# Kernel tuning notes

Measured on AMD Instinct MI355X. Metric: run time of the kernel, lower is better.

## Reference

```python
import jax, jax.numpy as jnp
import numpy as np

KNN, D, CONV_NUM, LEVELS, POOL_RATIO = 4, 64, 6, 3, 8
QN, RFN, NS, H, W = 4, 32, 4, 64, 64
CN = LEVELS * CONV_NUM  # 18 = 3 embed levels x 6 correlation variants


def instance_norm(x, eps=1e-5):
    # InstanceNorm2d(affine=False): normalize each (sample, channel) over H,W (biased var)
    m = x.mean(axis=(-2, -1), keepdims=True)
    v = x.var(axis=(-2, -1), keepdims=True)
    return (x - m) * jax.lax.rsqrt(v + eps)


def conv2d(x, w, b):
    y = jax.lax.conv_general_dilated(x, w, (1, 1), 'SAME', dimension_numbers=('NCHW', 'OIHW', 'NCHW'))
    return y + b[None, :, None, None]


def conv1x1x1(x, w, b):
    # Conv3d kernel 1x1x1 == pure channel mixing; x: (qn,C,ns,h,w), w: (Cout,Cin)
    return jnp.einsum('qcshw,oc->qoshw', x, w) + b[None, :, None, None, None]


def head(x, w1, b1, w2, b2, w3, b3):
    x = jax.nn.relu(conv2d(x, w1, b1))
    x = jax.nn.relu(conv2d(x, w2, b2))
    return conv2d(x, w3, b3)


def setup_inputs():
    key = jax.random.key(0)
    ks = iter(jax.random.split(key, 64))
    def rn(shape, scale=0.05):
        return jax.random.normal(next(ks), shape, jnp.float32) * scale
    inp = {'corr': jax.random.normal(next(ks), (QN, RFN, NS, CN, H, W), jnp.float32)}
    inp['scale_conv_w1'] = rn((D, CN * KNN)); inp['scale_conv_b1'] = rn((D,))
    inp['scale_conv_w2'] = rn((D, D)); inp['scale_conv_b2'] = rn((D,))
    inp['score_conv_w1'] = rn((D, LEVELS * KNN)); inp['score_conv_b1'] = rn((D,))
    inp['score_conv_w2'] = rn((D, D)); inp['score_conv_b2'] = rn((D,))
    for name, cout in (('scale_pred', 1), ('offset_pred', 2), ('score_pred', 1)):
        inp[name + '_w1'] = rn((D, D, 3, 3)); inp[name + '_b1'] = rn((D,))
        inp[name + '_w2'] = rn((D, D, 3, 3)); inp[name + '_b2'] = rn((D,))
        inp[name + '_w3'] = rn((cout, D, 3, 3)); inp[name + '_b3'] = rn((cout,))
    return inp


def _maps(corr, scale_conv_w1, scale_conv_b1, scale_conv_w2, scale_conv_b2,
          score_conv_w1, score_conv_b1, score_conv_w2, score_conv_b2,
          scale_pred_w1, scale_pred_b1, scale_pred_w2, scale_pred_b2, scale_pred_w3, scale_pred_b3,
          offset_pred_w1, offset_pred_b1, offset_pred_w2, offset_pred_b2, offset_pred_w3, offset_pred_b3,
          score_pred_w1, score_pred_b1, score_pred_w2, score_pred_b2, score_pred_w3, score_pred_b3):
    qn, rfn, ns, cn, h, w = corr.shape
    corr_n = instance_norm(corr)                         # score_norm
    # per-(scale,position) matching score per reference -> knn refs
    ref_score = corr_n.mean(axis=3)                      # qn,rfn,ns,h,w
    rs = jnp.moveaxis(ref_score, 1, -1)                  # qn,ns,h,w,rfn
    _, top_idx = jax.lax.top_k(rs, KNN)                  # qn,ns,h,w,knn
    feat = jnp.transpose(corr_n, (0, 2, 4, 5, 1, 3))     # qn,ns,h,w,rfn,cn
    knn_feat = jnp.take_along_axis(feat, top_idx[..., None], axis=4)  # qn,ns,h,w,knn,cn
    x_scale = jnp.transpose(knn_feat.reshape(qn, ns, h, w, KNN * cn), (0, 4, 1, 2, 3))  # qn,72,ns,h,w
    lvl = corr_n.reshape(qn, rfn, ns, LEVELS, CONV_NUM, h, w).mean(axis=4)  # per-level score
    lvl = jnp.transpose(lvl, (0, 2, 4, 5, 1, 3))         # qn,ns,h,w,rfn,3
    knn_lvl = jnp.take_along_axis(lvl, top_idx[..., None], axis=4)
    x_score = jnp.transpose(knn_lvl.reshape(qn, ns, h, w, KNN * LEVELS), (0, 4, 1, 2, 3))  # qn,12,ns,h,w
    xs = conv1x1x1(jax.nn.relu(conv1x1x1(x_scale, scale_conv_w1, scale_conv_b1)), scale_conv_w2, scale_conv_b2).max(axis=2)
    xc = conv1x1x1(jax.nn.relu(conv1x1x1(x_score, score_conv_w1, score_conv_b1)), score_conv_w2, score_conv_b2).max(axis=2)
    scales = head(xs, scale_pred_w1, scale_pred_b1, scale_pred_w2, scale_pred_b2, scale_pred_w3, scale_pred_b3)
    offsets = head(xc, offset_pred_w1, offset_pred_b1, offset_pred_w2, offset_pred_b2, offset_pred_w3, offset_pred_b3)
    scores = head(xc, score_pred_w1, score_pred_b1, score_pred_w2, score_pred_b2, score_pred_w3, score_pred_b3)
    return scores, scales, offsets


def reference(corr, scale_conv_w1, scale_conv_b1, scale_conv_w2, scale_conv_b2,
              score_conv_w1, score_conv_b1, score_conv_w2, score_conv_b2,
              scale_pred_w1, scale_pred_b1, scale_pred_w2, scale_pred_b2, scale_pred_w3, scale_pred_b3,
              offset_pred_w1, offset_pred_b1, offset_pred_w2, offset_pred_b2, offset_pred_w3, offset_pred_b3,
              score_pred_w1, score_pred_b1, score_pred_w2, score_pred_b2, score_pred_w3, score_pred_b3):
    scores, scales, offsets = _maps(corr, scale_conv_w1, scale_conv_b1, scale_conv_w2, scale_conv_b2,
                                    score_conv_w1, score_conv_b1, score_conv_w2, score_conv_b2,
                                    scale_pred_w1, scale_pred_b1, scale_pred_w2, scale_pred_b2, scale_pred_w3, scale_pred_b3,
                                    offset_pred_w1, offset_pred_b1, offset_pred_w2, offset_pred_b2, offset_pred_w3, offset_pred_b3,
                                    score_pred_w1, score_pred_b1, score_pred_w2, score_pred_b2, score_pred_w3, score_pred_b3)
    # parse_detection: argmax + advanced-index gathers
    qn = scores.shape[0]; h, w = scores.shape[-2:]
    sid = jnp.argmax(scores.reshape(qn, -1), axis=1)
    sy, sx = sid // w, sid % w
    q = jnp.arange(qn)
    off = offsets[q, :, sy, sx]                          # qn,2
    pos = (jnp.stack([sx, sy], -1).astype(scores.dtype) + off + 0.5) * POOL_RATIO - 0.5
    scl = 2.0 ** scales[q, 0, sy, sx]
    return pos, scl, scores, scales, offsets
```

## Files before the change

kernel.cpp:

```cpp
#include <hip/hip_runtime.h>

#define HW 4096

__global__ __launch_bounds__(256) void k_statsrs(
    const float* __restrict__ corr, float* __restrict__ scl,
    float* __restrict__ shf, float* __restrict__ rs,
    const float* __restrict__ p0, const float* __restrict__ p1,
    const float* __restrict__ p2, const float* __restrict__ p3,
    const float* __restrict__ p4, const float* __restrict__ p5,
    float* __restrict__ wT, const float* __restrict__ w1s,
    const float* __restrict__ w2s, const float* __restrict__ w1c,
    const float* __restrict__ w2c, float* __restrict__ wm) {
  int t = threadIdx.x;
  if (blockIdx.x >= 512) {
    int b = blockIdx.x - 512;
    if (b < 96) {
      int arr = b >> 4;
      int chunk = b & 15;
      const float* src = (arr == 0) ? p0
                         : (arr == 1) ? p1
                         : (arr == 2) ? p2
                         : (arr == 3) ? p3
                         : (arr == 4) ? p4 : p5;
      float* dst = wT + arr * 36864;
#pragma unroll
      for (int i = 0; i < 9; i++) {
        int e = chunk * 2304 + i * 256 + t;
        int oc = e / 576;
        int rem = e - oc * 576;
        dst[rem * 64 + oc] = src[e];
      }
    } else {
      int i = (b - 96) * 256 + t;
      if (i < 4608) {
        int c = i >> 6, o = i & 63;
        wm[i] = w1s[o * 72 + c];
      } else if (i < 8704) {
        int j = i - 4608;
        int c = j >> 6, o = j & 63;
        wm[i] = w2s[o * 64 + c];
      } else if (i < 9472) {
        int j = i - 8704;
        int c = j >> 6, o = j & 63;
        wm[i] = w1c[o * 12 + c];
      } else if (i < 13568) {
        int j = i - 9472;
        int c = j >> 6, o = j & 63;
        wm[i] = w2c[o * 64 + c];
      }
    }
    return;
  }
  int g = blockIdx.x;
  const float4* p = (const float4*)(corr + (size_t)g * 18 * HW);

  float s[18], s2[18];
#pragma unroll
  for (int c = 0; c < 18; c++) { s[c] = 0.f; s2[c] = 0.f; }
#pragma unroll
  for (int c = 0; c < 18; c++) {
#pragma unroll
    for (int i = 0; i < 4; i++) {
      float4 v = p[(c << 10) + (i << 8) + t];
      s[c] += v.x + v.y + v.z + v.w;
      s2[c] += v.x * v.x + v.y * v.y + v.z * v.z + v.w * v.w;
    }
  }
#pragma unroll
  for (int c = 0; c < 18; c++) {
#pragma unroll
    for (int o = 1; o < 64; o <<= 1) {
      s[c] += __shfl_xor(s[c], o, 64);
      s2[c] += __shfl_xor(s2[c], o, 64);
    }
  }
  __shared__ float lds_s[4][18], lds_s2[4][18];
  __shared__ float lds_scl[18], lds_shf[18];
  int wid = t >> 6;
  int ln = t & 63;
  if (ln < 18) {
    float vs = 0.f, vs2 = 0.f;
#pragma unroll
    for (int c = 0; c < 18; c++) {
      vs = (ln == c) ? s[c] : vs;
      vs2 = (ln == c) ? s2[c] : vs2;
    }
    lds_s[wid][ln] = vs;
    lds_s2[wid][ln] = vs2;
  }
  __syncthreads();
  if (t < 18) {
    float S = lds_s[0][t] + lds_s[1][t] + lds_s[2][t] + lds_s[3][t];
    float S2 = lds_s2[0][t] + lds_s2[1][t] + lds_s2[2][t] + lds_s2[3][t];
    float m = S * (1.f / HW);
    float var = S2 * (1.f / HW) - m * m;
    float r = rsqrtf(var + 1e-5f);
    scl[g * 18 + t] = r;
    shf[g * 18 + t] = -m * r;
    lds_scl[t] = r;
    lds_shf[t] = -m * r;
  }
  __syncthreads();

  float shsum = 0.f;
#pragma unroll
  for (int c = 0; c < 18; c++) shsum += lds_shf[c];
  const float inv = 1.f / 18.f;
#pragma unroll
  for (int i = 0; i < 4; i++) {
    float4 acc = make_float4(0.f, 0.f, 0.f, 0.f);
#pragma unroll
    for (int c = 0; c < 18; c++) {
      float4 v = p[(c << 10) + (i << 8) + t];
      float sc = lds_scl[c];
      acc.x = fmaf(v.x, sc, acc.x);
      acc.y = fmaf(v.y, sc, acc.y);
      acc.z = fmaf(v.z, sc, acc.z);
      acc.w = fmaf(v.w, sc, acc.w);
    }
    float4 o;
    o.x = (acc.x + shsum) * inv;
    o.y = (acc.y + shsum) * inv;
    o.z = (acc.z + shsum) * inv;
    o.w = (acc.w + shsum) * inv;
    ((float4*)(rs + (size_t)g * HW))[(i << 8) + t] = o;
  }
}

__global__ __launch_bounds__(256) void k_topk(const float* __restrict__ rs,
                                              int* __restrict__ topidx) {
  __shared__ float st[32 * 256];
  int b = blockIdx.x;
  int pxc = b & 15;
  int ns = (b >> 4) & 3;
  int q = b >> 6;
  int t = threadIdx.x;
  int pxb = pxc * 256;
#pragma unroll 8
  for (int r = 0; r < 32; r++)
    st[r * 256 + t] = rs[((q * 32 + r) * 4 + ns) * HW + pxb + t];
  __syncthreads();
  float v[32];
#pragma unroll
  for (int r = 0; r < 32; r++) v[r] = st[r * 256 + t];
  unsigned mask = 0;
  int sel[4];
#pragma unroll
  for (int k = 0; k < 4; k++) {
    float best = -3.4e38f;
    int bi = 0;
#pragma unroll
    for (int r = 0; r < 32; r++) {
      bool take = (!(mask & (1u << r))) && (v[r] > best);
      best = take ? v[r] : best;
      bi = take ? r : bi;
    }
    sel[k] = bi;
    mask |= (1u << bi);
  }
  ((int4*)topidx)[(q * 4 + ns) * HW + pxb + t] =
      make_int4(sel[0], sel[1], sel[2], sel[3]);
}

__global__ __launch_bounds__(256) void k_gather(const float* __restrict__ corr,
                                                const float* __restrict__ scl,
                                                const float* __restrict__ shf,
                                                const int* __restrict__ topidx,
                                                float* __restrict__ vbuf) {
  __shared__ float ls[32], lsh[32];
  int b = blockIdx.x;
  int c = b % 18;
  int rest = b / 18;
  int ns = rest & 3;
  int pxc = (rest >> 2) & 15;
  int q = rest >> 6;
  int t = threadIdx.x;
  int px = pxc * 256 + t;

  if (t < 32) {
    int g = q * 2304 + t * 72 + ns * 18 + c;
    ls[t] = scl[g];
    lsh[t] = shf[g];
  }
  int4 ti = ((const int4*)topidx)[(q * 4 + ns) * HW + px];
  int rk0 = ti.x, rk1 = ti.y, rk2 = ti.z, rk3 = ti.w;
  __syncthreads();

  const float* base = corr + (size_t)(((q * 32) * 4 + ns) * 18 + c) * HW + px;
  float v0 = 0.f, v1 = 0.f, v2 = 0.f, v3 = 0.f;
#pragma unroll
  for (int r = 0; r < 32; r++) {
    float x = base[(size_t)r * 72 * HW];
    v0 = (rk0 == r) ? x : v0;
    v1 = (rk1 == r) ? x : v1;
    v2 = (rk2 == r) ? x : v2;
    v3 = (rk3 == r) ? x : v3;
  }
  v0 = v0 * ls[rk0] + lsh[rk0];
  v1 = v1 * ls[rk1] + lsh[rk1];
  v2 = v2 * ls[rk2] + lsh[rk2];
  v3 = v3 * ls[rk3] + lsh[rk3];
  size_t ob = (size_t)((q * 4 + ns) * 72 + c) * HW + px;
  vbuf[ob] = v0;
  vbuf[ob + 18 * HW] = v1;
  vbuf[ob + 36 * HW] = v2;
  vbuf[ob + 54 * HW] = v3;
}

__global__ __launch_bounds__(256, 4) void k_mlp2(
    const float* __restrict__ vbuf, const float* __restrict__ wm,
    const float* __restrict__ b1s, const float* __restrict__ b2s,
    const float* __restrict__ b1c, const float* __restrict__ b2c,
    float* __restrict__ xs, float* __restrict__ xc) {
  __shared__ float lx[72 * 64];
  __shared__ float lh[64 * 64];
  __shared__ float lxsc[12 * 64];
  int blk = blockIdx.x;
  int q = blk >> 8, pxg = blk & 255;
  int t = threadIdx.x;
  int wi = t & 63;
  int oseg = t >> 6;
  int px0 = pxg * 16;

  const float* vq = vbuf + (size_t)(q * 4) * 72 * HW + px0;
#pragma unroll
  for (int j = 0; j < 18; j++) {
    int e = j * 256 + t;
    int c = e >> 6;
    int w2 = e & 63;
    int nns = w2 >> 4, ppx = w2 & 15;
    lx[c * 64 + w2] = vq[(size_t)(nns * 72 + c) * HW + ppx];
  }
  __syncthreads();

#pragma unroll
  for (int m = 0; m < 3; m++) {
    int idx = m * 256 + t;
    int l = idx >> 6, w2 = idx & 63;
    float sm = 0.f;
#pragma unroll
    for (int j = 0; j < 6; j++) sm += lx[(l * 6 + j) * 64 + w2];
    lxsc[l * 64 + w2] = sm * (1.f / 6.f);
  }

  float h[16];
  const float* bp1 = b1s + oseg * 16;
#pragma unroll
  for (int o = 0; o < 16; o++) h[o] = bp1[o];
#pragma unroll
  for (int c = 0; c < 72; c++) {
    float x = lx[c * 64 + wi];
    const float* wr = wm + c * 64 + oseg * 16;
#pragma unroll
    for (int o = 0; o < 16; o++) h[o] = fmaf(wr[o], x, h[o]);
  }
#pragma unroll
  for (int o = 0; o < 16; o++) lh[(oseg * 16 + o) * 64 + wi] = fmaxf(h[o], 0.f);
  __syncthreads();

  float a[16];
  const float* bp2 = b2s + oseg * 16;
#pragma unroll
  for (int o = 0; o < 16; o++) a[o] = bp2[o];
#pragma unroll
  for (int c = 0; c < 64; c++) {
    float x = lh[c * 64 + wi];
    const float* wr = wm + 4608 + c * 64 + oseg * 16;
#pragma unroll
    for (int o = 0; o < 16; o++) a[o] = fmaf(wr[o], x, a[o]);
  }
#pragma unroll
  for (int o = 0; o < 16; o++) lx[(oseg * 16 + o) * 64 + wi] = a[o];
  __syncthreads();

#pragma unroll
  for (int m = 0; m < 4; m++) {
    int idx = m * 256 + t;
    int oc = idx >> 4, ppx = idx & 15;
    float v = lx[oc * 64 + ppx];
    v = fmaxf(v, lx[oc * 64 + 16 + ppx]);
    v = fmaxf(v, lx[oc * 64 + 32 + ppx]);
    v = fmaxf(v, lx[oc * 64 + 48 + ppx]);
    xs[(size_t)(q * 64 + oc) * HW + px0 + ppx] = v;
  }

  const float* bc1 = b1c + oseg * 16;
#pragma unroll
  for (int o = 0; o < 16; o++) h[o] = bc1[o];
#pragma unroll
  for (int c = 0; c < 12; c++) {
    float x = lxsc[c * 64 + wi];
    const float* wr = wm + 8704 + c * 64 + oseg * 16;
#pragma unroll
    for (int o = 0; o < 16; o++) h[o] = fmaf(wr[o], x, h[o]);
  }
  __syncthreads();
#pragma unroll
  for (int o = 0; o < 16; o++) lh[(oseg * 16 + o) * 64 + wi] = fmaxf(h[o], 0.f);
  __syncthreads();

  const float* bc2 = b2c + oseg * 16;
#pragma unroll
  for (int o = 0; o < 16; o++) a[o] = bc2[o];
#pragma unroll
  for (int c = 0; c < 64; c++) {
    float x = lh[c * 64 + wi];
    const float* wr = wm + 9472 + c * 64 + oseg * 16;
#pragma unroll
    for (int o = 0; o < 16; o++) a[o] = fmaf(wr[o], x, a[o]);
  }
#pragma unroll
  for (int o = 0; o < 16; o++) lx[(oseg * 16 + o) * 64 + wi] = a[o];
  __syncthreads();

#pragma unroll
  for (int m = 0; m < 4; m++) {
    int idx = m * 256 + t;
    int oc = idx >> 4, ppx = idx & 15;
    float v = lx[oc * 64 + ppx];
    v = fmaxf(v, lx[oc * 64 + 16 + ppx]);
    v = fmaxf(v, lx[oc * 64 + 32 + ppx]);
    v = fmaxf(v, lx[oc * 64 + 48 + ppx]);
    xc[(size_t)(q * 64 + oc) * HW + px0 + ppx] = v;
  }
}

template <bool RELU>
__global__ __launch_bounds__(256) void k_conv3h(
    const float* __restrict__ in0, const float* __restrict__ in1,
    const float* __restrict__ in2, const float* __restrict__ w0,
    const float* __restrict__ w1, const float* __restrict__ w2,
    const float* __restrict__ bb0, const float* __restrict__ bb1,
    const float* __restrict__ bb2, float* __restrict__ o0,
    float* __restrict__ o1, float* __restrict__ o2) {
  __shared__ float tile[16 * 10 * 72];
  int b = blockIdx.x;
  int hi = b >> 5;
  int og = hi / 3;
  int head = hi - og * 3;
  int q = (b >> 3) & 3;
  int rt = b & 7;
  const float* in = head == 0 ? in0 : head == 1 ? in1 : in2;
  const float* wT = head == 0 ? w0 : head == 1 ? w1 : w2;
  const float* bb = head == 0 ? bb0 : head == 1 ? bb1 : bb2;
  float* outp = head == 0 ? o0 : head == 1 ? o1 : o2;

  int t = threadIdx.x;
  int w = t & 63;
  int wr = t >> 6;
  int lane4 = t & 15;
  int rgrp = t >> 4;
  float acc[2][16];
#pragma unroll
  for (int pr = 0; pr < 2; pr++)
#pragma unroll
    for (int o = 0; o < 16; o++) acc[pr][o] = 0.f;
  const float* inq = in + (size_t)q * 64 * HW;

  for (int icc = 0; icc < 4; icc++) {
    __syncthreads();
    if (t < 160) { tile[t * 72 + 3] = 0.f; tile[t * 72 + 68] = 0.f; }
#pragma unroll
    for (int p = 0; p < 10; p++) {
      int idx = p * 16 + rgrp;
      int ch = idx / 10;
      int r = idx - ch * 10;
      int grow = rt * 8 + r - 1;
      float4 val = make_float4(0.f, 0.f, 0.f, 0.f);
      if (grow >= 0 && grow < 64)
        val = *(const float4*)(inq + (size_t)(icc * 16 + ch) * HW + grow * 64 +
                               lane4 * 4);
      *(float4*)(tile + idx * 72 + 4 + lane4 * 4) = val;
    }
    __syncthreads();
#pragma unroll 2
    for (int ic = 0; ic < 16; ic++) {
      float xv[4][3];
      const float* tb = tile + (ic * 10 + wr * 2) * 72 + w + 3;
#pragma unroll
      for (int rr = 0; rr < 4; rr++)
#pragma unroll
        for (int dc = 0; dc < 3; dc++) xv[rr][dc] = tb[rr * 72 + dc];
      const float* wb = wT + (size_t)(icc * 16 + ic) * 9 * 64 + og * 16;
#pragma unroll
      for (int dr = 0; dr < 3; dr++)
#pragma unroll
        for (int dc = 0; dc < 3; dc++) {
          const float* wv = wb + (dr * 3 + dc) * 64;
#pragma unroll
          for (int o = 0; o < 16; o++) {
            float wj = wv[o];
            acc[0][o] = fmaf(wj, xv[0 + dr][dc], acc[0][o]);
            acc[1][o] = fmaf(wj, xv[1 + dr][dc], acc[1][o]);
          }
        }
    }
  }
#pragma unroll
  for (int pr = 0; pr < 2; pr++) {
    int orow = rt * 8 + wr * 2 + pr;
#pragma unroll
    for (int o = 0; o < 16; o++) {
      float rz = acc[pr][o] + bb[og * 16 + o];
      if (RELU) rz = fmaxf(rz, 0.f);
      outp[((size_t)q * 64 + og * 16 + o) * HW + orow * 64 + w] = rz;
    }
  }
}

__global__ __launch_bounds__(256) void k_convSh(
    const float* __restrict__ in0, const float* __restrict__ in1,
    const float* __restrict__ in2, const float* __restrict__ wt0,
    const float* __restrict__ wt1, const float* __restrict__ wt2,
    const float* __restrict__ bb0, const float* __restrict__ bb1,
    const float* __restrict__ bb2, float* __restrict__ o0,
    float* __restrict__ o1, float* __restrict__ o2) {
  __shared__ float tile[64 * 3 * 66];
  __shared__ float red[4 * 2 * 64];
  int b = blockIdx.x;
  int head = b >> 8;
  int q = (b >> 6) & 3;
  int row = b & 63;
  const float* in = head == 0 ? in0 : head == 1 ? in1 : in2;
  const float* wt = head == 0 ? wt0 : head == 1 ? wt1 : wt2;
  const float* bb = head == 0 ? bb0 : head == 1 ? bb1 : bb2;
  float* outp = head == 0 ? o0 : head == 1 ? o1 : o2;
  int noc = (head == 1) ? 2 : 1;

  int t = threadIdx.x;
  int w = t & 63;
  int sub = t >> 6;
  if (t < 192) { tile[t * 66] = 0.f; tile[t * 66 + 65] = 0.f; }
  __syncthreads();
  const float* inq = in + (size_t)q * 64 * HW;
#pragma unroll
  for (int i = 0; i < 48; i++) {
    int idx = i * 4 + sub;
    int ic = idx / 3;
    int r = idx - ic * 3;
    int grow = row + r - 1;
    float val = 0.f;
    if (grow >= 0 && grow < 64) val = inq[(size_t)ic * HW + grow * 64 + w];
    tile[idx * 66 + 1 + w] = val;
  }
  __syncthreads();
  float acc0 = 0.f, acc1 = 0.f;
#pragma unroll 4
  for (int i = 0; i < 16; i++) {
    int ic = sub * 16 + i;
    float x[9];
#pragma unroll
    for (int dr = 0; dr < 3; dr++)
#pragma unroll
      for (int dc = 0; dc < 3; dc++)
        x[dr * 3 + dc] = tile[(ic * 3 + dr) * 66 + w + dc];
    const float* wb = wt + (size_t)ic * 9;
#pragma unroll
    for (int j = 0; j < 9; j++) acc0 += wb[j] * x[j];
    if (noc == 2) {
      const float* wb1 = wt + 576 + (size_t)ic * 9;
#pragma unroll
      for (int j = 0; j < 9; j++) acc1 += wb1[j] * x[j];
    }
  }
  red[(sub * 2 + 0) * 64 + w] = acc0;
  if (noc == 2) red[(sub * 2 + 1) * 64 + w] = acc1;
  __syncthreads();
  if (t < 128) {
    int o = t >> 6;
    if (o < noc) {
      float s = red[(0 * 2 + o) * 64 + w] + red[(1 * 2 + o) * 64 + w] +
                red[(2 * 2 + o) * 64 + w] + red[(3 * 2 + o) * 64 + w] + bb[o];
      outp[((size_t)q * noc + o) * HW + row * 64 + w] = s;
    }
  }
}

__global__ __launch_bounds__(256) void k_final(const float* __restrict__ scores,
                                               const float* __restrict__ scales,
                                               const float* __restrict__ offsets,
                                               float* __restrict__ pos,
                                               float* __restrict__ sclo) {
  int q = blockIdx.x, t = threadIdx.x;
  float best = -3.4e38f;
  int bi = 1 << 30;
  for (int i = t; i < HW; i += 256) {
    float v = scores[q * HW + i];
    if (v > best) { best = v; bi = i; }
  }
  __shared__ float bv[256];
  __shared__ int bix[256];
  bv[t] = best;
  bix[t] = bi;
  __syncthreads();
  for (int s = 128; s > 0; s >>= 1) {
    if (t < s) {
      if (bv[t + s] > bv[t] || (bv[t + s] == bv[t] && bix[t + s] < bix[t])) {
        bv[t] = bv[t + s];
        bix[t] = bix[t + s];
      }
    }
    __syncthreads();
  }
  if (t == 0) {
    int sid = bix[0];
    int sy = sid >> 6, sx = sid & 63;
    float o0 = offsets[(q * 2 + 0) * HW + sid];
    float o1 = offsets[(q * 2 + 1) * HW + sid];
    pos[q * 2 + 0] = ((float)sx + o0 + 0.5f) * 8.f - 0.5f;
    pos[q * 2 + 1] = ((float)sy + o1 + 0.5f) * 8.f - 0.5f;
    sclo[q] = exp2f(scales[q * HW + sid]);
  }
}

extern "C" void kernel_launch(void* const* d_in, const int* in_sizes, int n_in,
                              void* d_out, int out_size, void* d_ws, size_t ws_size,
                              hipStream_t stream) {
  const float* corr = (const float*)d_in[0];
  const float* w1s = (const float*)d_in[1];
  const float* b1s = (const float*)d_in[2];
  const float* w2s = (const float*)d_in[3];
  const float* b2s = (const float*)d_in[4];
  const float* w1c = (const float*)d_in[5];
  const float* b1c = (const float*)d_in[6];
  const float* w2c = (const float*)d_in[7];
  const float* b2c = (const float*)d_in[8];

  float* out = (float*)d_out;
  float* pos = out;
  float* sclo = out + 8;
  float* scores = out + 12;
  float* scales = out + 12 + 16384;
  float* offsets = out + 12 + 32768;

  char* ws = (char*)d_ws;
  float* st_scl = (float*)(ws + 0);
  float* st_shf = (float*)(ws + 36864);
  int* topidx = (int*)(ws + 73728);
  float* rs = (float*)(ws + 1122304);
  float* vbuf = rs;
  float* wT = (float*)(ws + 19996672);
  float* wmT = (float*)(ws + 20881408);
  float* xs = (float*)(ws + 20971520);
  float* xc = (float*)(ws + 25165824);
  float* t1s = vbuf;
  float* t1o = (float*)((char*)vbuf + 4194304);
  float* t1c = (float*)((char*)vbuf + 8388608);
  float* t2c = (float*)((char*)vbuf + 12582912);
  float* t2s = xs;
  float* t2o = xc;

  k_statsrs<<<661, 256, 0, stream>>>(
      corr, st_scl, st_shf, rs, (const float*)d_in[9], (const float*)d_in[11],
      (const float*)d_in[15], (const float*)d_in[17], (const float*)d_in[21],
      (const float*)d_in[23], wT, w1s, w2s, w1c, w2c, wmT);
  k_topk<<<256, 256, 0, stream>>>(rs, topidx);
  k_gather<<<4608, 256, 0, stream>>>(corr, st_scl, st_shf, topidx, vbuf);
  k_mlp2<<<1024, 256, 0, stream>>>(vbuf, wmT, b1s, b2s, b1c, b2c, xs, xc);
  k_conv3h<true><<<384, 256, 0, stream>>>(
      xs, xc, xc, wT, wT + 2 * 36864, wT + 4 * 36864,
      (const float*)d_in[10], (const float*)d_in[16], (const float*)d_in[22],
      t1s, t1o, t1c);
  k_conv3h<true><<<384, 256, 0, stream>>>(
      t1s, t1o, t1c, wT + 1 * 36864, wT + 3 * 36864, wT + 5 * 36864,
      (const float*)d_in[12], (const float*)d_in[18], (const float*)d_in[24],
      t2s, t2o, t2c);
  k_convSh<<<768, 256, 0, stream>>>(
      t2s, t2o, t2c, (const float*)d_in[13], (const float*)d_in[19],
      (const float*)d_in[25], (const float*)d_in[14], (const float*)d_in[20],
      (const float*)d_in[26], scales, offsets, scores);

  k_final<<<4, 256, 0, stream>>>(scores, scales, offsets, pos, sclo);
}
```

Baseline: 600.5 us.

## Fuse top-k gather into MLP kernel and widen blocks to 512 threads

```diff
diff --git a/kernel.cpp b/kernel.cpp
--- a/kernel.cpp
+++ b/kernel.cpp
@@ -162,56 +162,13 @@
       make_int4(sel[0], sel[1], sel[2], sel[3]);
 }
 
-__global__ __launch_bounds__(256) void k_gather(const float* __restrict__ corr,
-                                                const float* __restrict__ scl,
-                                                const float* __restrict__ shf,
-                                                const int* __restrict__ topidx,
-                                                float* __restrict__ vbuf) {
-  __shared__ float ls[32], lsh[32];
-  int b = blockIdx.x;
-  int c = b % 18;
-  int rest = b / 18;
-  int ns = rest & 3;
-  int pxc = (rest >> 2) & 15;
-  int q = rest >> 6;
-  int t = threadIdx.x;
-  int px = pxc * 256 + t;
-
-  if (t < 32) {
-    int g = q * 2304 + t * 72 + ns * 18 + c;
-    ls[t] = scl[g];
-    lsh[t] = shf[g];
-  }
-  int4 ti = ((const int4*)topidx)[(q * 4 + ns) * HW + px];
-  int rk0 = ti.x, rk1 = ti.y, rk2 = ti.z, rk3 = ti.w;
-  __syncthreads();
-
-  const float* base = corr + (size_t)(((q * 32) * 4 + ns) * 18 + c) * HW + px;
-  float v0 = 0.f, v1 = 0.f, v2 = 0.f, v3 = 0.f;
-#pragma unroll
-  for (int r = 0; r < 32; r++) {
-    float x = base[(size_t)r * 72 * HW];
-    v0 = (rk0 == r) ? x : v0;
-    v1 = (rk1 == r) ? x : v1;
-    v2 = (rk2 == r) ? x : v2;
-    v3 = (rk3 == r) ? x : v3;
-  }
-  v0 = v0 * ls[rk0] + lsh[rk0];
-  v1 = v1 * ls[rk1] + lsh[rk1];
-  v2 = v2 * ls[rk2] + lsh[rk2];
-  v3 = v3 * ls[rk3] + lsh[rk3];
-  size_t ob = (size_t)((q * 4 + ns) * 72 + c) * HW + px;
-  vbuf[ob] = v0;
-  vbuf[ob + 18 * HW] = v1;
-  vbuf[ob + 36 * HW] = v2;
-  vbuf[ob + 54 * HW] = v3;
-}
-
-__global__ __launch_bounds__(256, 4) void k_mlp2(
-    const float* __restrict__ vbuf, const float* __restrict__ wm,
-    const float* __restrict__ b1s, const float* __restrict__ b2s,
-    const float* __restrict__ b1c, const float* __restrict__ b2c,
-    float* __restrict__ xs, float* __restrict__ xc) {
+__global__ __launch_bounds__(512, 8) void k_mlp3(
+    const float* __restrict__ corr, const float* __restrict__ scl,
+    const float* __restrict__ shf, const int* __restrict__ topidx,
+    const float* __restrict__ wm, const float* __restrict__ b1s,
+    const float* __restrict__ b2s, const float* __restrict__ b1c,
+    const float* __restrict__ b2c, float* __restrict__ xs,
+    float* __restrict__ xc) {
   __shared__ float lx[72 * 64];
   __shared__ float lh[64 * 64];
   __shared__ float lxsc[12 * 64];
@@ -220,108 +177,119 @@
   int t = threadIdx.x;
   int wi = t & 63;
   int oseg = t >> 6;
-  int px0 = pxg * 16;
-
-  const float* vq = vbuf + (size_t)(q * 4) * 72 * HW + px0;
-#pragma unroll
-  for (int j = 0; j < 18; j++) {
-    int e = j * 256 + t;
-    int c = e >> 6;
-    int w2 = e & 63;
-    int nns = w2 >> 4, ppx = w2 & 15;
-    lx[c * 64 + w2] = vq[(size_t)(nns * 72 + c) * HW + ppx];
-  }
-  __syncthreads();
-
-#pragma unroll
-  for (int m = 0; m < 3; m++) {
-    int idx = m * 256 + t;
-    int l = idx >> 6, w2 = idx & 63;
-    float sm = 0.f;
-#pragma unroll
-    for (int j = 0; j < 6; j++) sm += lx[(l * 6 + j) * 64 + w2];
-    lxsc[l * 64 + w2] = sm * (1.f / 6.f);
-  }
-
-  float h[16];
-  const float* bp1 = b1s + oseg * 16;
-#pragma unroll
-  for (int o = 0; o < 16; o++) h[o] = bp1[o];
+  int ns = (t >> 4) & 3;
+  int pxi = t & 15;
+  int px = pxg * 16 + pxi;
+  int k = oseg >> 1;
+  int ch0 = (oseg & 1) * 9;
+
+  int4 ti = ((const int4*)topidx)[(q * 4 + ns) * HW + px];
+  int rk = (k == 0) ? ti.x : (k == 1) ? ti.y : (k == 2) ? ti.z : ti.w;
+  int gidx = ((q * 32 + rk) * 4 + ns) * 18 + ch0;
+  const float* cb = corr + (size_t)gidx * HW + px;
+  const float* sb = scl + gidx;
+  const float* hb = shf + gidx;
+  float xv[9], sv[9], hv[9];
+#pragma unroll
+  for (int j = 0; j < 9; j++) xv[j] = cb[(size_t)j * HW];
+#pragma unroll
+  for (int j = 0; j < 9; j++) sv[j] = sb[j];
+#pragma unroll
+  for (int j = 0; j < 9; j++) hv[j] = hb[j];
+#pragma unroll
+  for (int j = 0; j < 9; j++)
+    lx[(k * 18 + ch0 + j) * 64 + wi] = fmaf(xv[j], sv[j], hv[j]);
+  __syncthreads();
+
+#pragma unroll
+  for (int m = 0; m < 2; m++) {
+    int idx = m * 512 + t;
+    if (idx < 768) {
+      int l = idx >> 6, w2 = idx & 63;
+      float sm = 0.f;
+#pragma unroll
+      for (int j = 0; j < 6; j++) sm += lx[(l * 6 + j) * 64 + w2];
+      lxsc[l * 64 + w2] = sm * (1.f / 6.f);
+    }
+  }
+
+  float h[8];
+  const float* bp1 = b1s + oseg * 8;
+#pragma unroll
+  for (int o = 0; o < 8; o++) h[o] = bp1[o];
 #pragma unroll
   for (int c = 0; c < 72; c++) {
     float x = lx[c * 64 + wi];
-    const float* wr = wm + c * 64 + oseg * 16;
-#pragma unroll
-    for (int o = 0; o < 16; o++) h[o] = fmaf(wr[o], x, h[o]);
-  }
-#pragma unroll
-  for (int o = 0; o < 16; o++) lh[(oseg * 16 + o) * 64 + wi] = fmaxf(h[o], 0.f);
-  __syncthreads();
-
-  float a[16];
-  const float* bp2 = b2s + oseg * 16;
-#pragma unroll
-  for (int o = 0; o < 16; o++) a[o] = bp2[o];
+    const float* wr = wm + c * 64 + oseg * 8;
+#pragma unroll
+    for (int o = 0; o < 8; o++) h[o] = fmaf(wr[o], x, h[o]);
+  }
+#pragma unroll
+  for (int o = 0; o < 8; o++) lh[(oseg * 8 + o) * 64 + wi] = fmaxf(h[o], 0.f);
+  __syncthreads();
+
+  float a[8];
+  const float* bp2 = b2s + oseg * 8;
+#pragma unroll
+  for (int o = 0; o < 8; o++) a[o] = bp2[o];
 #pragma unroll
   for (int c = 0; c < 64; c++) {
     float x = lh[c * 64 + wi];
-    const float* wr = wm + 4608 + c * 64 + oseg * 16;
-#pragma unroll
-    for (int o = 0; o < 16; o++) a[o] = fmaf(wr[o], x, a[o]);
-  }
-#pragma unroll
-  for (int o = 0; o < 16; o++) lx[(oseg * 16 + o) * 64 + wi] = a[o];
-  __syncthreads();
-
-#pragma unroll
-  for (int m = 0; m < 4; m++) {
-    int idx = m * 256 + t;
+    const float* wr = wm + 4608 + c * 64 + oseg * 8;
+#pragma unroll
+    for (int o = 0; o < 8; o++) a[o] = fmaf(wr[o], x, a[o]);
+  }
+#pragma unroll
+  for (int o = 0; o < 8; o++) lx[(oseg * 8 + o) * 64 + wi] = a[o];
+  __syncthreads();
+
+#pragma unroll
+  for (int m = 0; m < 2; m++) {
+    int idx = m * 512 + t;
     int oc = idx >> 4, ppx = idx & 15;
     float v = lx[oc * 64 + ppx];
     v = fmaxf(v, lx[oc * 64 + 16 + ppx]);
     v = fmaxf(v, lx[oc * 64 + 32 + ppx]);
     v = fmaxf(v, lx[oc * 64 + 48 + ppx]);
-    xs[(size_t)(q * 64 + oc) * HW + px0 + ppx] = v;
-  }
-
-  const float* bc1 = b1c + oseg * 16;
-#pragma unroll
-  for (int o = 0; o < 16; o++) h[o] = bc1[o];
+    xs[(size_t)(q * 64 + oc) * HW + pxg * 16 + ppx] = v;
+  }
+  const float* bc1 = b1c + oseg * 8;
+#pragma unroll
+  for (int o = 0; o < 8; o++) h[o] = bc1[o];
 #pragma unroll
   for (int c = 0; c < 12; c++) {
     float x = lxsc[c * 64 + wi];
-    const float* wr = wm + 8704 + c * 64 + oseg * 16;
-#pragma unroll
-    for (int o = 0; o < 16; o++) h[o] = fmaf(wr[o], x, h[o]);
-  }
-  __syncthreads();
-#pragma unroll
-  for (int o = 0; o < 16; o++) lh[(oseg * 16 + o) * 64 + wi] = fmaxf(h[o], 0.f);
-  __syncthreads();
-
-  const float* bc2 = b2c + oseg * 16;
-#pragma unroll
-  for (int o = 0; o < 16; o++) a[o] = bc2[o];
+    const float* wr = wm + 8704 + c * 64 + oseg * 8;
+#pragma unroll
+    for (int o = 0; o < 8; o++) h[o] = fmaf(wr[o], x, h[o]);
+  }
+#pragma unroll
+  for (int o = 0; o < 8; o++) lh[(oseg * 8 + o) * 64 + wi] = fmaxf(h[o], 0.f);
+  __syncthreads();
+
+  const float* bc2 = b2c + oseg * 8;
+#pragma unroll
+  for (int o = 0; o < 8; o++) a[o] = bc2[o];
 #pragma unroll
   for (int c = 0; c < 64; c++) {
     float x = lh[c * 64 + wi];
-    const float* wr = wm + 9472 + c * 64 + oseg * 16;
-#pragma unroll
-    for (int o = 0; o < 16; o++) a[o] = fmaf(wr[o], x, a[o]);
-  }
-#pragma unroll
-  for (int o = 0; o < 16; o++) lx[(oseg * 16 + o) * 64 + wi] = a[o];
-  __syncthreads();
-
-#pragma unroll
-  for (int m = 0; m < 4; m++) {
-    int idx = m * 256 + t;
+    const float* wr = wm + 9472 + c * 64 + oseg * 8;
+#pragma unroll
+    for (int o = 0; o < 8; o++) a[o] = fmaf(wr[o], x, a[o]);
+  }
+#pragma unroll
+  for (int o = 0; o < 8; o++) lx[(oseg * 8 + o) * 64 + wi] = a[o];
+  __syncthreads();
+
+#pragma unroll
+  for (int m = 0; m < 2; m++) {
+    int idx = m * 512 + t;
     int oc = idx >> 4, ppx = idx & 15;
     float v = lx[oc * 64 + ppx];
     v = fmaxf(v, lx[oc * 64 + 16 + ppx]);
     v = fmaxf(v, lx[oc * 64 + 32 + ppx]);
     v = fmaxf(v, lx[oc * 64 + 48 + ppx]);
-    xc[(size_t)(q * 64 + oc) * HW + px0 + ppx] = v;
+    xc[(size_t)(q * 64 + oc) * HW + pxg * 16 + ppx] = v;
   }
 }
 
@@ -538,15 +506,14 @@
   float* st_shf = (float*)(ws + 36864);
   int* topidx = (int*)(ws + 73728);
   float* rs = (float*)(ws + 1122304);
-  float* vbuf = rs;
   float* wT = (float*)(ws + 19996672);
   float* wmT = (float*)(ws + 20881408);
   float* xs = (float*)(ws + 20971520);
   float* xc = (float*)(ws + 25165824);
-  float* t1s = vbuf;
-  float* t1o = (float*)((char*)vbuf + 4194304);
-  float* t1c = (float*)((char*)vbuf + 8388608);
-  float* t2c = (float*)((char*)vbuf + 12582912);
+  float* t1s = rs;
+  float* t1o = (float*)((char*)rs + 4194304);
+  float* t1c = (float*)((char*)rs + 8388608);
+  float* t2c = (float*)((char*)rs + 12582912);
   float* t2s = xs;
   float* t2o = xc;
 
@@ -555,8 +522,8 @@
       (const float*)d_in[15], (const float*)d_in[17], (const float*)d_in[21],
       (const float*)d_in[23], wT, w1s, w2s, w1c, w2c, wmT);
   k_topk<<<256, 256, 0, stream>>>(rs, topidx);
-  k_gather<<<4608, 256, 0, stream>>>(corr, st_scl, st_shf, topidx, vbuf);
-  k_mlp2<<<1024, 256, 0, stream>>>(vbuf, wmT, b1s, b2s, b1c, b2c, xs, xc);
+  k_mlp3<<<1024, 512, 0, stream>>>(corr, st_scl, st_shf, topidx, wmT, b1s, b2s,
+                                   b1c, b2c, xs, xc);
   k_conv3h<true><<<384, 256, 0, stream>>>(
       xs, xc, xc, wT, wT + 2 * 36864, wT + 4 * 36864,
       (const float*)d_in[10], (const float*)d_in[16], (const float*)d_in[22],
```

Measured after the change: 600.2 us. About the same (-0.1%).
